# Kernel optimization log

Hardware: AMD Instinct MI355X
Metric: run time of the kernel (lower is better)

Reference implementation:

```python
import jax, jax.numpy as jnp
import numpy as np

N_NODES = 100000
N_EDGES = 1600000
F_IN, HID, N_CLS = 64, 64, 40
K = 3  # Chebyshev order


def setup_inputs() -> dict:
    key = jax.random.key(0)
    k = jax.random.split(key, 7)
    x = jax.random.normal(k[0], (N_NODES, F_IN), dtype=jnp.float32)
    edge_index = jax.random.randint(k[1], (2, N_EDGES), 0, N_NODES, dtype=jnp.int32)
    W1 = jax.random.normal(k[2], (K, F_IN, HID), dtype=jnp.float32) * 0.05
    b1 = jax.random.normal(k[3], (HID,), dtype=jnp.float32) * 0.05
    W2 = jax.random.normal(k[4], (K, HID, N_CLS), dtype=jnp.float32) * 0.05
    b2 = jax.random.normal(k[5], (N_CLS,), dtype=jnp.float32) * 0.05
    return {"x": x, "edge_index": edge_index, "W1": W1, "b1": b1, "W2": W2, "b2": b2}


def _norm(edge_index, n):
    # PyG ChebConv with sym normalization and lambda_max=2.0:
    # L_hat edge weight = -deg^{-1/2}[src] * deg^{-1/2}[dst]; self-loop weight 0.
    src, dst = edge_index[0], edge_index[1]
    keep = (src != dst).astype(jnp.float32)  # remove_self_loops
    deg = jax.ops.segment_sum(keep, src, num_segments=n)
    dis = jnp.where(deg > 0, 1.0 / jnp.sqrt(jnp.maximum(deg, 1.0)), 0.0)
    w = -dis[src] * dis[dst] * keep
    return src, dst, w


def _spmm(x, src, dst, w, n):
    # out[i] = sum_{e: dst[e]==i} w[e] * x[src[e]]
    return jax.ops.segment_sum(w[:, None] * x[src], dst, num_segments=n)


def _cheb_conv(x, src, dst, w, W, b, n):
    Tx0 = x
    out = Tx0 @ W[0]
    Tx1 = _spmm(x, src, dst, w, n)
    out = out + Tx1 @ W[1]
    for k in range(2, W.shape[0]):
        Tx2 = 2.0 * _spmm(Tx1, src, dst, w, n) - Tx0
        out = out + Tx2 @ W[k]
        Tx0, Tx1 = Tx1, Tx2
    return out + b


def reference(x, edge_index, W1, b1, W2, b2):
    n = x.shape[0]
    src, dst, w = _norm(edge_index, n)
    h = jax.nn.relu(_cheb_conv(x, src, dst, w, W1, b1, n))
    out = _cheb_conv(h, src, dst, w, W2, b2, n)
    return jax.nn.softmax(out, axis=1)
```

## Files before the change

kernel.cpp:

```cpp
#include <hip/hip_runtime.h>
#include <hip/hip_fp16.h>

#define N_NODES 100000
#define N_EDGES 1600000
#define NCLS 40
#define NBUCK 196
#define CAPE 8960
#define CAPC 10752
#define DUMMY N_NODES

typedef unsigned short u16;
typedef unsigned int u32;
typedef short bf16x8 __attribute__((ext_vector_type(8)));
typedef float f32x4 __attribute__((ext_vector_type(4)));

static inline size_t align256(size_t x) { return (x + 255) & ~(size_t)255; }

__device__ __forceinline__ float bf2f(u16 h) { return __uint_as_float(((u32)h) << 16); }
__device__ __forceinline__ u16 f2bf(float f) {
    u32 u = __float_as_uint(f);
    u += 0x7FFFu + ((u >> 16) & 1u);
    return (u16)(u >> 16);
}
__device__ __forceinline__ u32 pk2(u16 a, u16 b) { return (u32)a | ((u32)b << 16); }
__device__ __forceinline__ u32 pack15(float f) {
    return ((u32)__half_as_ushort(__float2half(f))) & 0x7FFFu;
}
__device__ __forceinline__ float unpack15(u32 bits) {
    return __half2float(__ushort_as_half((u16)bits));
}

#define PS_BLOCKS 391
#define CONV_BLOCKS 6250

__global__ __launch_bounds__(256) void pscatter_conv(const int* __restrict__ src,
                                                     const int* __restrict__ dst,
                                                     int* __restrict__ gFillD,
                                                     int* __restrict__ gFillS,
                                                     u32* __restrict__ partD,
                                                     int* __restrict__ partS,
                                                     const float* __restrict__ x,
                                                     u16* __restrict__ xb) {
    if (blockIdx.x >= PS_BLOCKS) {
        int i = (blockIdx.x - PS_BLOCKS) * 256 + threadIdx.x;
        float4 v = *(const float4*)(x + (size_t)i * 4);
        ushort4 o;
        o.x = f2bf(v.x); o.y = f2bf(v.y); o.z = f2bf(v.z); o.w = f2bf(v.w);
        *(ushort4*)(xb + (size_t)i * 4) = o;
        return;
    }
    __shared__ int histD[NBUCK], histS[NBUCK], chunkD[NBUCK], chunkS[NBUCK];
    int tid = threadIdx.x;
    int base = blockIdx.x * 4096;

    int4 sv[4], dv[4];
#pragma unroll
    for (int j = 0; j < 4; ++j) {
        int idx = base + j * 1024 + tid * 4;
        if (idx < N_EDGES) {
            sv[j] = *(const int4*)(src + idx);
            dv[j] = *(const int4*)(dst + idx);
        } else {
            sv[j] = make_int4(0, 0, 0, 0);
            dv[j] = make_int4(0, 0, 0, 0);
        }
    }

    for (int i = tid; i < NBUCK; i += 256) { histD[i] = 0; histS[i] = 0; }
    __syncthreads();
#pragma unroll
    for (int j = 0; j < 4; ++j)
#pragma unroll
        for (int k = 0; k < 4; ++k) {
            int s = ((const int*)&sv[j])[k], d = ((const int*)&dv[j])[k];
            if (s != d) {
                atomicAdd(&histD[d >> 9], 1);
                atomicAdd(&histS[s >> 9], 1);
            }
        }
    __syncthreads();
    for (int B = tid; B < NBUCK; B += 256) {
        int cD = histD[B];
        chunkD[B] = cD ? atomicAdd(&gFillD[B], cD) : 0;
        int cS = histS[B];
        chunkS[B] = cS ? atomicAdd(&gFillS[B], cS) : 0;
    }
    __syncthreads();
    for (int i = tid; i < NBUCK; i += 256) { histD[i] = 0; histS[i] = 0; }
    __syncthreads();
#pragma unroll
    for (int j = 0; j < 4; ++j)
#pragma unroll
        for (int k = 0; k < 4; ++k) {
            int s = ((const int*)&sv[j])[k], d = ((const int*)&dv[j])[k];
            if (s != d) {
                int bD = d >> 9;
                int r = atomicAdd(&histD[bD], 1);
                int o = chunkD[bD] + r;
                if (o < CAPE) partD[bD * CAPE + o] = ((u32)s << 9) | (u32)(d & 511);
                int bS = s >> 9;
                int r2 = atomicAdd(&histS[bS], 1);
                int o2 = chunkS[bS] + r2;
                if (o2 < CAPE) partS[bS * CAPE + o2] = s;
            }
        }
}

__global__ __launch_bounds__(256) void build_dis(const int* __restrict__ partS,
                                                 const int* __restrict__ gFillS,
                                                 float* __restrict__ dis) {
    __shared__ int cnt[512];
    int tid = threadIdx.x;
    int B = blockIdx.x;
    for (int i = tid; i < 512; i += 256) cnt[i] = 0;
    __syncthreads();
    int nS = min(gFillS[B], CAPE);
    for (int i = tid; i < nS; i += 256) atomicAdd(&cnt[partS[B * CAPE + i] & 511], 1);
    __syncthreads();
    for (int n = tid; n < 512; n += 256) {
        int node = B * 512 + n;
        if (node < N_NODES) {
            int dg = cnt[n];
            dis[node] = dg > 0 ? 1.0f / sqrtf((float)dg) : 0.0f;
        }
    }
}

__global__ __launch_bounds__(256) void build_csr(const u32* __restrict__ partD,
                                                 const int* __restrict__ gFillD,
                                                 const float* __restrict__ dis,
                                                 u32* __restrict__ csr,
                                                 int2* __restrict__ meta) {
    __shared__ int cnt[512], loc[512], rnk[512];
    int tid = threadIdx.x;
    int B = blockIdx.x;
    for (int i = tid; i < 512; i += 256) { cnt[i] = 0; rnk[i] = 0; }
    __syncthreads();
    int nD = min(gFillD[B], CAPE);
    for (int i = tid; i < nD; i += 256) atomicAdd(&cnt[partD[B * CAPE + i] & 511], 1);
    __syncthreads();
    if (tid < 64) {
        int bb = tid * 8, c8[8], mysum = 0;
#pragma unroll
        for (int j = 0; j < 8; ++j) { c8[j] = (cnt[bb + j] + 7) & ~7; mysum += c8[j]; }
        int incl = mysum;
#pragma unroll
        for (int off = 1; off < 64; off <<= 1) {
            int v = __shfl_up(incl, off);
            if (tid >= off) incl += v;
        }
        int run = incl - mysum;
#pragma unroll
        for (int j = 0; j < 8; ++j) { loc[bb + j] = run; run += c8[j]; }
    }
    __syncthreads();
    for (int n = tid; n < 512; n += 256) {
        int node = B * 512 + n;
        if (node < N_NODES) {
            meta[node] = make_int2(B * CAPC + loc[n], cnt[n]);
            int c = cnt[n], c8 = (c + 7) & ~7;
            for (int e = c; e < c8; ++e) csr[B * CAPC + loc[n] + e] = (u32)DUMMY;
        }
    }
    for (int i = tid; i < nD; i += 256) {
        u32 p = partD[B * CAPE + i];
        int ln = p & 511;
        u32 s = p >> 9;
        int r = atomicAdd(&rnk[ln], 1);
        int pos = loc[ln] + r;
        if (pos < CAPC) csr[B * CAPC + pos] = s | (pack15(dis[s]) << 17);
    }
}

__global__ __launch_bounds__(256) void spmm(const u16* __restrict__ in,
                                            const float* __restrict__ dis,
                                            const int2* __restrict__ meta,
                                            const u32* __restrict__ csr,
                                            u16* __restrict__ outhi,
                                            u16* __restrict__ outlo) {
    int node = (blockIdx.x * 256 + threadIdx.x) >> 6;
    int lane = threadIdx.x & 63;
    if (node >= N_NODES) return;
    int2 mt = meta[node];
    int c8 = (mt.y + 7) & ~7;
    const u32* lst = csr + mt.x;
    const u32* in32 = (const u32*)in;
    const int hsel = lane >> 5;
    const int fl = lane & 31;
    float acc0 = 0.0f, acc1 = 0.0f;
    int e = 0;
    for (; e + 16 <= c8; e += 16) {
        uint4 ea = *(const uint4*)(lst + e);
        uint4 eb = *(const uint4*)(lst + e + 4);
        uint4 ec = *(const uint4*)(lst + e + 8);
        uint4 ed = *(const uint4*)(lst + e + 12);
        u32 e0 = hsel ? ea.y : ea.x;
        u32 e1 = hsel ? ea.w : ea.z;
        u32 e2 = hsel ? eb.y : eb.x;
        u32 e3 = hsel ? eb.w : eb.z;
        u32 e4 = hsel ? ec.y : ec.x;
        u32 e5 = hsel ? ec.w : ec.z;
        u32 e6 = hsel ? ed.y : ed.x;
        u32 e7 = hsel ? ed.w : ed.z;
        u32 v0 = in32[((e0 & 0x1FFFFu) << 5) + fl];
        u32 v1 = in32[((e1 & 0x1FFFFu) << 5) + fl];
        u32 v2 = in32[((e2 & 0x1FFFFu) << 5) + fl];
        u32 v3 = in32[((e3 & 0x1FFFFu) << 5) + fl];
        u32 v4 = in32[((e4 & 0x1FFFFu) << 5) + fl];
        u32 v5 = in32[((e5 & 0x1FFFFu) << 5) + fl];
        u32 v6 = in32[((e6 & 0x1FFFFu) << 5) + fl];
        u32 v7 = in32[((e7 & 0x1FFFFu) << 5) + fl];
        float w0 = unpack15(e0 >> 17), w1 = unpack15(e1 >> 17);
        float w2 = unpack15(e2 >> 17), w3 = unpack15(e3 >> 17);
        float w4 = unpack15(e4 >> 17), w5 = unpack15(e5 >> 17);
        float w6 = unpack15(e6 >> 17), w7 = unpack15(e7 >> 17);
        acc0 = fmaf(w0, __uint_as_float(v0 << 16), acc0);
        acc1 = fmaf(w0, __uint_as_float(v0 & 0xFFFF0000u), acc1);
        acc0 = fmaf(w1, __uint_as_float(v1 << 16), acc0);
        acc1 = fmaf(w1, __uint_as_float(v1 & 0xFFFF0000u), acc1);
        acc0 = fmaf(w2, __uint_as_float(v2 << 16), acc0);
        acc1 = fmaf(w2, __uint_as_float(v2 & 0xFFFF0000u), acc1);
        acc0 = fmaf(w3, __uint_as_float(v3 << 16), acc0);
        acc1 = fmaf(w3, __uint_as_float(v3 & 0xFFFF0000u), acc1);
        acc0 = fmaf(w4, __uint_as_float(v4 << 16), acc0);
        acc1 = fmaf(w4, __uint_as_float(v4 & 0xFFFF0000u), acc1);
        acc0 = fmaf(w5, __uint_as_float(v5 << 16), acc0);
        acc1 = fmaf(w5, __uint_as_float(v5 & 0xFFFF0000u), acc1);
        acc0 = fmaf(w6, __uint_as_float(v6 << 16), acc0);
        acc1 = fmaf(w6, __uint_as_float(v6 & 0xFFFF0000u), acc1);
        acc0 = fmaf(w7, __uint_as_float(v7 << 16), acc0);
        acc1 = fmaf(w7, __uint_as_float(v7 & 0xFFFF0000u), acc1);
    }
    if (e < c8) {
        uint4 ea = *(const uint4*)(lst + e);
        uint4 eb = *(const uint4*)(lst + e + 4);
        u32 e0 = hsel ? ea.y : ea.x;
        u32 e1 = hsel ? ea.w : ea.z;
        u32 e2 = hsel ? eb.y : eb.x;
        u32 e3 = hsel ? eb.w : eb.z;
        u32 v0 = in32[((e0 & 0x1FFFFu) << 5) + fl];
        u32 v1 = in32[((e1 & 0x1FFFFu) << 5) + fl];
        u32 v2 = in32[((e2 & 0x1FFFFu) << 5) + fl];
        u32 v3 = in32[((e3 & 0x1FFFFu) << 5) + fl];
        float w0 = unpack15(e0 >> 17), w1 = unpack15(e1 >> 17);
        float w2 = unpack15(e2 >> 17), w3 = unpack15(e3 >> 17);
        acc0 = fmaf(w0, __uint_as_float(v0 << 16), acc0);
        acc1 = fmaf(w0, __uint_as_float(v0 & 0xFFFF0000u), acc1);
        acc0 = fmaf(w1, __uint_as_float(v1 << 16), acc0);
        acc1 = fmaf(w1, __uint_as_float(v1 & 0xFFFF0000u), acc1);
        acc0 = fmaf(w2, __uint_as_float(v2 << 16), acc0);
        acc1 = fmaf(w2, __uint_as_float(v2 & 0xFFFF0000u), acc1);
        acc0 = fmaf(w3, __uint_as_float(v3 << 16), acc0);
        acc1 = fmaf(w3, __uint_as_float(v3 & 0xFFFF0000u), acc1);
    }
    acc0 += __shfl_xor(acc0, 32);
    acc1 += __shfl_xor(acc1, 32);
    float vd = -dis[node];
    float f0 = vd * acc0, f1 = vd * acc1;
    u32 o32 = ((u32)node << 5) + fl;
    u16 h0 = f2bf(f0), h1 = f2bf(f1);
    if (hsel == 0) {
        ((u32*)outhi)[o32] = pk2(h0, h1);
    } else {
        ((u32*)outlo)[o32] = pk2(f2bf(f0 - bf2f(h0)), f2bf(f1 - bf2f(h1)));
    }
}

#define DGRID 625
#define DNT 10
#define LSTR 200

__device__ __forceinline__ float foldW(const float* __restrict__ W, int kk, int col,
                                       int ncols) {
    float wv = W[kk * ncols + col];
    if (kk < 64) wv -= W[(kk + 128) * ncols + col];
    else if (kk >= 128) wv += wv;
    return wv;
}

__global__ __launch_bounds__(256) void dense1_mf(const float* __restrict__ x,
                                                 const u16* __restrict__ a1h,
                                                 const u16* __restrict__ a1l,
                                                 const u16* __restrict__ tyh,
                                                 const u16* __restrict__ tyl,
                                                 const float* __restrict__ W,
                                                 const float* __restrict__ bias,
                                                 u16* __restrict__ ohi,
                                                 u16* __restrict__ olo) {
    __shared__ u16 Ah[16 * LSTR], Al[16 * LSTR];
    const int tid = threadIdx.x, wid = tid >> 6, lane = tid & 63;
    const int lrow = lane & 15, lk8 = (lane >> 4) * 8;
    const int col = wid * 16 + lrow;

    bf16x8 wh[6], wl[6];
#pragma unroll
    for (int c = 0; c < 6; ++c) {
        bf16x8 h, l;
#pragma unroll
        for (int i = 0; i < 8; ++i) {
            float wv = foldW(W, c * 32 + lk8 + i, col, 64);
            u16 hb_ = f2bf(wv);
            h[i] = (short)hb_;
            l[i] = (short)f2bf(wv - bf2f(hb_));
        }
        wh[c] = h; wl[c] = l;
    }
    float bv = bias[col];
    const int srow = tid >> 4, sc4 = (tid & 15) * 4;

    for (int t = 0; t < DNT; ++t) {
        int r0 = (blockIdx.x * DNT + t) * 16;
        size_t rb = ((size_t)(r0 + srow) << 6) + sc4;
        {
            float4 v = *(const float4*)&x[rb];
            const float* vp = (const float*)&v;
            ushort4 hv, lv;
#pragma unroll
            for (int i = 0; i < 4; ++i) {
                u16 hb_ = f2bf(vp[i]);
                ((u16*)&hv)[i] = hb_;
                ((u16*)&lv)[i] = f2bf(vp[i] - bf2f(hb_));
            }
            *(ushort4*)&Ah[srow * LSTR + sc4] = hv;
            *(ushort4*)&Al[srow * LSTR + sc4] = lv;
        }
        *(ushort4*)&Ah[srow * LSTR + 64 + sc4] = *(const ushort4*)&a1h[rb];
        *(ushort4*)&Al[srow * LSTR + 64 + sc4] = *(const ushort4*)&a1l[rb];
        *(ushort4*)&Ah[srow * LSTR + 128 + sc4] = *(const ushort4*)&tyh[rb];
        *(ushort4*)&Al[srow * LSTR + 128 + sc4] = *(const ushort4*)&tyl[rb];
        __syncthreads();

        f32x4 acc = {bv, bv, bv, bv};
#pragma unroll
        for (int c = 0; c < 6; ++c) {
            bf16x8 ah = *(const bf16x8*)&Ah[lrow * LSTR + c * 32 + lk8];
            bf16x8 al = *(const bf16x8*)&Al[lrow * LSTR + c * 32 + lk8];
            acc = __builtin_amdgcn_mfma_f32_16x16x32_bf16(ah, wh[c], acc, 0, 0, 0);
            acc = __builtin_amdgcn_mfma_f32_16x16x32_bf16(al, wh[c], acc, 0, 0, 0);
            acc = __builtin_amdgcn_mfma_f32_16x16x32_bf16(ah, wl[c], acc, 0, 0, 0);
        }
        __syncthreads();

#pragma unroll
        for (int j = 0; j < 4; ++j) {
            int row = r0 + (lane >> 4) * 4 + j;
            float v = fmaxf(acc[j], 0.0f);
            u16 hb_ = f2bf(v);
            ohi[((size_t)row << 6) + col] = hb_;
            olo[((size_t)row << 6) + col] = f2bf(v - bf2f(hb_));
        }
    }
}

__global__ __launch_bounds__(256) void dense2_mf(const u16* __restrict__ a0h,
                                                 const u16* __restrict__ a0l,
                                                 const u16* __restrict__ a1h,
                                                 const u16* __restrict__ a1l,
                                                 const u16* __restrict__ tyh,
                                                 const u16* __restrict__ tyl,
                                                 const float* __restrict__ W,
                                                 const float* __restrict__ bias,
                                                 float* __restrict__ out) {
    __shared__ u16 Ah[16 * LSTR], Al[16 * LSTR];
    __shared__ float Ls[16][48];
    const int tid = threadIdx.x, wid = tid >> 6, lane = tid & 63;
    const int lrow = lane & 15, lk8 = (lane >> 4) * 8;
    const int col = wid * 16 + lrow;
    const bool act = (wid < 3);
    const bool cok = act && (col < NCLS);

    bf16x8 wh[6], wl[6];
#pragma unroll
    for (int c = 0; c < 6; ++c) {
        bf16x8 h = 0, l = 0;
        if (cok) {
#pragma unroll
            for (int i = 0; i < 8; ++i) {
                float wv = foldW(W, c * 32 + lk8 + i, col, NCLS);
                u16 hb_ = f2bf(wv);
                h[i] = (short)hb_;
                l[i] = (short)f2bf(wv - bf2f(hb_));
            }
        }
        wh[c] = h; wl[c] = l;
    }
    float bv = cok ? bias[col] : 0.0f;
    const int srow = tid >> 4, sc4 = (tid & 15) * 4;

    for (int t = 0; t < DNT; ++t) {
        int r0 = (blockIdx.x * DNT + t) * 16;
        size_t rb = ((size_t)(r0 + srow) << 6) + sc4;
        *(ushort4*)&Ah[srow * LSTR + sc4] = *(const ushort4*)&a0h[rb];
        *(ushort4*)&Al[srow * LSTR + sc4] = *(const ushort4*)&a0l[rb];
        *(ushort4*)&Ah[srow * LSTR + 64 + sc4] = *(const ushort4*)&a1h[rb];
        *(ushort4*)&Al[srow * LSTR + 64 + sc4] = *(const ushort4*)&a1l[rb];
        *(ushort4*)&Ah[srow * LSTR + 128 + sc4] = *(const ushort4*)&tyh[rb];
        *(ushort4*)&Al[srow * LSTR + 128 + sc4] = *(const ushort4*)&tyl[rb];
        __syncthreads();

        if (act) {
            f32x4 acc = {bv, bv, bv, bv};
#pragma unroll
            for (int c = 0; c < 6; ++c) {
                bf16x8 ah = *(const bf16x8*)&Ah[lrow * LSTR + c * 32 + lk8];
                bf16x8 al = *(const bf16x8*)&Al[lrow * LSTR + c * 32 + lk8];
                acc = __builtin_amdgcn_mfma_f32_16x16x32_bf16(ah, wh[c], acc, 0, 0, 0);
                acc = __builtin_amdgcn_mfma_f32_16x16x32_bf16(al, wh[c], acc, 0, 0, 0);
                acc = __builtin_amdgcn_mfma_f32_16x16x32_bf16(ah, wl[c], acc, 0, 0, 0);
            }
#pragma unroll
            for (int j = 0; j < 4; ++j) Ls[(lane >> 4) * 4 + j][col] = acc[j];
        }
        __syncthreads();

        {
            int row = wid * 4 + (lane >> 4);
            int cg = lane & 15;
            float v0 = Ls[row][cg];
            float v1 = Ls[row][cg + 16];
            float v2 = (cg < 8) ? Ls[row][cg + 32] : -1e30f;
            float m = fmaxf(fmaxf(v0, v1), v2);
#pragma unroll
            for (int o = 8; o; o >>= 1) m = fmaxf(m, __shfl_xor(m, o));
            float e0 = expf(v0 - m), e1 = expf(v1 - m);
            float e2 = (cg < 8) ? expf(v2 - m) : 0.0f;
            float s = e0 + e1 + e2;
#pragma unroll
            for (int o = 8; o; o >>= 1) s += __shfl_xor(s, o);
            float inv = 1.0f / s;
            size_t ob = (size_t)(r0 + row) * NCLS;
            out[ob + cg] = e0 * inv;
            out[ob + cg + 16] = e1 * inv;
            if (cg < 8) out[ob + cg + 32] = e2 * inv;
        }
    }
}


extern "C" void kernel_launch(void* const* d_in, const int* in_sizes, int n_in,
                              void* d_out, int out_size, void* d_ws, size_t ws_size,
                              hipStream_t stream) {
    const float* x = (const float*)d_in[0];
    const int* edge_index = (const int*)d_in[1];
    const float* W1 = (const float*)d_in[2];
    const float* b1 = (const float*)d_in[3];
    const float* W2 = (const float*)d_in[4];
    const float* b2 = (const float*)d_in[5];
    float* out = (float*)d_out;

    const int* src = edge_index;
    const int* dst = edge_index + N_EDGES;

    char* ws = (char*)d_ws;
    size_t off = 0;
    auto carve = [&](size_t bytes) -> void* {
        void* p = ws + off;
        off = align256(off + bytes);
        return p;
    };
    int* gFillD = (int*)carve((size_t)NBUCK * 4);
    int* gFillS = (int*)carve((size_t)NBUCK * 4);
    size_t zero_bytes = off;
    u32* partD = (u32*)carve((size_t)NBUCK * CAPE * 4);
    int* partS = (int*)carve((size_t)NBUCK * CAPE * 4);
    u32* csr = (u32*)carve((size_t)NBUCK * CAPC * 4 + 1024);
    int2* meta = (int2*)carve((size_t)N_NODES * 8);
    float* dis = (float*)carve((size_t)(N_NODES + 1) * 4);
    const size_t FB = (size_t)(N_NODES + 1) * 64 * 2;
    u16* xb  = (u16*)carve(FB);
    u16* t1h = (u16*)carve(FB);
    u16* t1l = (u16*)carve(FB);
    u16* tyh = (u16*)carve(FB);
    u16* tyl = (u16*)carve(FB);
    u16* hh  = (u16*)carve(FB);
    u16* hl  = (u16*)carve(FB);

    const int WV = (N_NODES * 64) / 256;

    hipMemsetAsync(d_ws, 0, zero_bytes, stream);
    hipMemsetAsync(dis + N_NODES, 0, 4, stream);
    hipMemsetAsync(xb + (size_t)N_NODES * 64, 0, 128, stream);
    hipMemsetAsync(t1h + (size_t)N_NODES * 64, 0, 128, stream);
    hipMemsetAsync(hh + (size_t)N_NODES * 64, 0, 128, stream);

    pscatter_conv<<<PS_BLOCKS + CONV_BLOCKS, 256, 0, stream>>>(src, dst, gFillD, gFillS,
                                                               partD, partS, x, xb);
    build_dis<<<NBUCK, 256, 0, stream>>>(partS, gFillS, dis);
    build_csr<<<NBUCK, 256, 0, stream>>>(partD, gFillD, dis, csr, meta);

    spmm<<<WV, 256, 0, stream>>>(xb, dis, meta, csr, t1h, t1l);
    spmm<<<WV, 256, 0, stream>>>(t1h, dis, meta, csr, tyh, tyl);
    dense1_mf<<<DGRID, 256, 0, stream>>>(x, t1h, t1l, tyh, tyl, W1, b1, hh, hl);

    spmm<<<WV, 256, 0, stream>>>(hh, dis, meta, csr, t1h, t1l);
    spmm<<<WV, 256, 0, stream>>>(t1h, dis, meta, csr, tyh, tyl);
    dense2_mf<<<DGRID, 256, 0, stream>>>(hh, hl, t1h, t1l, tyh, tyl, W2, b2, out);
}
```

Measured before the change: 276.7 us.

## Permute CSR edge order so each half-wave loads contiguous edges; retune dense grid

The CSR build now stores edges in a permuted order within each 16-edge (or 8-edge tail) group, so even and odd edges sit in separate contiguous halves. Each half-wave in spmm can then read its 8 edges with two uint4 loads instead of reading all 16 and selecting. This halves edge-list load traffic per lane and removes the select instructions, at the cost of an extra index computation in the build. Separately, the dense kernel grid is doubled while tiles per block are halved, trading more blocks for less work each.

```diff
diff --git a/kernel.cpp b/kernel.cpp
--- a/kernel.cpp
+++ b/kernel.cpp
@@ -28,6 +28,15 @@
 }
 __device__ __forceinline__ float unpack15(u32 bits) {
     return __half2float(__ushort_as_half((u16)bits));
+}
+__device__ __forceinline__ int perm16(int r, int c8) {
+    int base16 = (c8 >> 4) << 4;
+    if (r < base16) {
+        int b = r >> 4, w = r & 15;
+        return (b << 4) + ((w & 1) << 3) + (w >> 1);
+    }
+    int w = r - base16;
+    return base16 + ((w & 1) << 2) + (w >> 1);
 }
 
 #define PS_BLOCKS 391
@@ -157,9 +166,10 @@
     for (int n = tid; n < 512; n += 256) {
         int node = B * 512 + n;
         if (node < N_NODES) {
-            meta[node] = make_int2(B * CAPC + loc[n], cnt[n]);
             int c = cnt[n], c8 = (c + 7) & ~7;
-            for (int e = c; e < c8; ++e) csr[B * CAPC + loc[n] + e] = (u32)DUMMY;
+            meta[node] = make_int2(B * CAPC + loc[n], c);
+            for (int e = c; e < c8; ++e)
+                csr[B * CAPC + loc[n] + perm16(e, c8)] = (u32)DUMMY;
         }
     }
     for (int i = tid; i < nD; i += 256) {
@@ -167,7 +177,8 @@
         int ln = p & 511;
         u32 s = p >> 9;
         int r = atomicAdd(&rnk[ln], 1);
-        int pos = loc[ln] + r;
+        int c8 = (cnt[ln] + 7) & ~7;
+        int pos = loc[ln] + perm16(r, c8);
         if (pos < CAPC) csr[B * CAPC + pos] = s | (pack15(dis[s]) << 17);
     }
 }
@@ -190,18 +201,11 @@
     float acc0 = 0.0f, acc1 = 0.0f;
     int e = 0;
     for (; e + 16 <= c8; e += 16) {
-        uint4 ea = *(const uint4*)(lst + e);
-        uint4 eb = *(const uint4*)(lst + e + 4);
-        uint4 ec = *(const uint4*)(lst + e + 8);
-        uint4 ed = *(const uint4*)(lst + e + 12);
-        u32 e0 = hsel ? ea.y : ea.x;
-        u32 e1 = hsel ? ea.w : ea.z;
-        u32 e2 = hsel ? eb.y : eb.x;
-        u32 e3 = hsel ? eb.w : eb.z;
-        u32 e4 = hsel ? ec.y : ec.x;
-        u32 e5 = hsel ? ec.w : ec.z;
-        u32 e6 = hsel ? ed.y : ed.x;
-        u32 e7 = hsel ? ed.w : ed.z;
+        const u32* half = lst + e + (hsel << 3);
+        uint4 ea = *(const uint4*)half;
+        uint4 eb = *(const uint4*)(half + 4);
+        u32 e0 = ea.x, e1 = ea.y, e2 = ea.z, e3 = ea.w;
+        u32 e4 = eb.x, e5 = eb.y, e6 = eb.z, e7 = eb.w;
         u32 v0 = in32[((e0 & 0x1FFFFu) << 5) + fl];
         u32 v1 = in32[((e1 & 0x1FFFFu) << 5) + fl];
         u32 v2 = in32[((e2 & 0x1FFFFu) << 5) + fl];
@@ -232,12 +236,9 @@
         acc1 = fmaf(w7, __uint_as_float(v7 & 0xFFFF0000u), acc1);
     }
     if (e < c8) {
-        uint4 ea = *(const uint4*)(lst + e);
-        uint4 eb = *(const uint4*)(lst + e + 4);
-        u32 e0 = hsel ? ea.y : ea.x;
-        u32 e1 = hsel ? ea.w : ea.z;
-        u32 e2 = hsel ? eb.y : eb.x;
-        u32 e3 = hsel ? eb.w : eb.z;
+        const u32* half = lst + e + (hsel << 2);
+        uint4 ea = *(const uint4*)half;
+        u32 e0 = ea.x, e1 = ea.y, e2 = ea.z, e3 = ea.w;
         u32 v0 = in32[((e0 & 0x1FFFFu) << 5) + fl];
         u32 v1 = in32[((e1 & 0x1FFFFu) << 5) + fl];
         u32 v2 = in32[((e2 & 0x1FFFFu) << 5) + fl];
@@ -266,8 +267,8 @@
     }
 }
 
-#define DGRID 625
-#define DNT 10
+#define DGRID 1250
+#define DNT 5
 #define LSTR 200
 
 __device__ __forceinline__ float foldW(const float* __restrict__ W, int kk, int col,
```

Result: faster. 270.6 us (-2.2%).
